# Kernel tuning notes

Measured on AMD Instinct MI355X. Metric: run time of the kernel, lower is better.

Reference implementation:

```python
import jax, jax.numpy as jnp
import numpy as np

B = 36          # fixed batch_size in source
T = 60          # time_window
DECAY = 0.3     # LIAF default decay
THRESH = 0.5    # LIAF default firing threshold


def conv3x3(x, W, b):
    # x: [B,C,H,W], W: [O,C,3,3], padding=1, stride=1
    y = jax.lax.conv_general_dilated(x, W, (1, 1), [(1, 1), (1, 1)],
                                     dimension_numbers=('NCHW', 'OIHW', 'NCHW'))
    return y + b[None, :, None, None]


def avgpool2(x):
    # 2x2 average pool, stride 2
    b, c, h, w = x.shape
    return x.reshape(b, c, h // 2, 2, w // 2, 2).mean(axis=(3, 5))


def liaf(u, spike, mem):
    # leaky-integrate with spike-gated reset, analog (ReLU) fire
    mem = mem * DECAY * (1.0 - spike) + u
    new_spike = (mem > THRESH).astype(mem.dtype)
    out = jax.nn.relu(mem)
    return new_spike, mem, out


def setup_inputs() -> dict:
    key = jax.random.key(0)
    ks = jax.random.split(key, 8)
    # DVS event frames in [0,3) so the >1 binarization keeps ~2/3 of pixels
    data = (jax.random.uniform(ks[0], (B, 2, 32, 32, T)) * 3.0).astype(jnp.float32)

    def w(k, shape, fan_in):
        return (jax.random.normal(k, shape) * (1.0 / np.sqrt(fan_in))).astype(jnp.float32)

    return dict(
        data=data,
        win=T,
        W0=w(ks[1], (64, 2, 3, 3), 2 * 9), b0=jnp.zeros((64,), jnp.float32),
        W1=w(ks[2], (128, 64, 3, 3), 64 * 9), b1=jnp.zeros((128,), jnp.float32),
        W2=w(ks[3], (128, 128, 3, 3), 128 * 9), b2=jnp.zeros((128,), jnp.float32),
        Wf1=w(ks[4], (256, 8192), 8192), bf1=jnp.zeros((256,), jnp.float32),
        Wf2=w(ks[5], (11, 256), 256), bf2=jnp.zeros((11,), jnp.float32),
    )


def reference(data, W0, b0, W1, b1, W2, b2, Wf1, bf1, Wf2, bf2, win):
    dtype = data.dtype
    z = lambda s: jnp.zeros(s, dtype)
    # (spike, mem) pairs for every LIAF cell + output-spike accumulator
    state0 = (
        (z((B, 64, 32, 32)), z((B, 64, 32, 32))),   # c0
        (z((B, 128, 32, 32)), z((B, 128, 32, 32))), # c1
        (z((B, 128, 16, 16)), z((B, 128, 16, 16))), # p1
        (z((B, 128, 16, 16)), z((B, 128, 16, 16))), # c2
        (z((B, 128, 8, 8)), z((B, 128, 8, 8))),     # p2
        (z((B, 256)), z((B, 256))),                 # h1
        (z((B, 11)), z((B, 11))),                   # h2
        z((B, 11)),                                 # sum of analog outputs
    )
    xs = jnp.moveaxis(data, -1, 0)[:win]

    def step(st, xt):
        c0, c1, p1, c2, p2, h1, h2, acc = st
        x = (xt > 1.0).astype(dtype)  # binarize accumulated frame
        s, m, out = liaf(conv3x3(x, W0, b0), *c0); c0 = (s, m)
        s, m, out = liaf(conv3x3(out, W1, b1), *c1); c1 = (s, m)
        s, m, out = liaf(avgpool2(out), *p1); p1 = (s, m)
        s, m, out = liaf(conv3x3(out, W2, b2), *c2); c2 = (s, m)
        s, m, out = liaf(avgpool2(out), *p2); p2 = (s, m)
        out = out.reshape(B, -1)  # [B, 8*8*128]
        s, m, out = liaf(out @ Wf1.T + bf1, *h1); h1 = (s, m)
        s, m, out = liaf(out @ Wf2.T + bf2, *h2); h2 = (s, m)
        return (c0, c1, p1, c2, p2, h1, h2, acc + out), None

    st_f, _ = jax.lax.scan(step, state0, xs)
    return st_f[-1] / T
```

## Files before the change

### kernel.cpp

```cpp
#include <hip/hip_runtime.h>

#define NB 36
#define NT 60

typedef __attribute__((ext_vector_type(8))) short short8;
typedef __attribute__((ext_vector_type(4))) float f32x4;

struct Params {
  const float *data;
  const float *W0, *b0, *W1, *b1, *W2, *b2, *Wf1, *bf1, *Wf2, *bf2;
  float *xb, *w0t;
  unsigned short *w1h, *w1l, *w2h, *w2l;
  unsigned int *xhl, *p1hl;
  float *outp2, *u1s;
  float *dm0, *dm1, *dmp1, *dm2, *dmp2, *dmh1, *dmh2;
  float *acc;
  float *zbase; int zn4;
};

__device__ __forceinline__ unsigned short bf16_rne(float v){
  unsigned int bits = __float_as_uint(v);
  unsigned int r = bits + 0x7FFFu + ((bits >> 16) & 1u);
  return (unsigned short)(r >> 16);
}
__device__ __forceinline__ unsigned int bf16pack(float v){
  unsigned short h = bf16_rne(v);
  float hf = __uint_as_float((unsigned int)h << 16);
  unsigned short l = bf16_rne(v - hf);
  return (unsigned int)h | ((unsigned int)l << 16);
}
__device__ __forceinline__ void unpack8(const unsigned int* q, short8& h8, short8& l8){
  unsigned int u[8];
  *(uint4*)&u[0] = *(const uint4*)q;
  *(uint4*)&u[4] = *(const uint4*)(q+4);
  #pragma unroll
  for(int i=0;i<8;i++){
    h8[i] = (short)(u[i] & 0xffffu);
    l8[i] = (short)(u[i] >> 16);
  }
}

__global__ void __launch_bounds__(256) k_prep(Params p){
  int gt  = blockIdx.x*256 + threadIdx.x;
  int STR = gridDim.x*256;
  if(gt < NB*11) p.acc[gt] = 0.f;
  for(int i=gt; i<p.zn4; i+=STR) ((float4*)p.zbase)[i] = make_float4(0.f,0.f,0.f,0.f);
  const int PLANE = 34*34;
  for(int i=gt; i<NT*NB*2*PLANE; i+=STR){
    int t   = i / (NB*2*PLANE);
    int rem = i % (NB*2*PLANE);
    int bc  = rem / PLANE;
    int pix = rem % PLANE;
    int ph = pix/34, pw = pix%34;
    float v = 0.f;
    if(ph>=1 && ph<=32 && pw>=1 && pw<=32){
      float d = p.data[((size_t)bc*1024 + (ph-1)*32 + (pw-1))*NT + t];
      v = (d > 1.0f) ? 1.0f : 0.0f;
    }
    p.xb[i] = v;
  }
  for(int i=gt; i<2*9*64; i+=STR){
    int co=i%64, rr=i/64; p.w0t[i] = p.W0[(co*2 + rr/9)*9 + rr%9];
  }
  for(int i=gt; i<128*576; i+=STR){
    int co = i/576, k = i%576;
    int cin = k/9, dd = k%9;
    unsigned int pk = bf16pack(p.W1[(co*64+cin)*9 + dd]);
    p.w1h[i]=(unsigned short)(pk&0xffffu); p.w1l[i]=(unsigned short)(pk>>16);
  }
  for(int i=gt; i<128*1152; i+=STR){
    int co = i/1152, k = i%1152;
    int cin = k/9, dd = k%9;
    unsigned int pk = bf16pack(p.W2[(co*128+cin)*9 + dd]);
    p.w2h[i]=(unsigned short)(pk&0xffffu); p.w2l[i]=(unsigned short)(pk>>16);
  }
}

template<int Cin,int Cout,int HW,int CO,int PX,int TY,int CS>
__global__ void __launch_bounds__(HW*TY)
k_conv0(const float* __restrict__ x, const float* __restrict__ wt,
        const float* __restrict__ bias, float* __restrict__ dm,
        unsigned int* __restrict__ outhl,
        const float* __restrict__ u1s, const float* __restrict__ bf1,
        const float* __restrict__ Wf2, const float* __restrict__ bf2,
        float* __restrict__ dmh1, float* __restrict__ dmh2,
        float* __restrict__ accv, int do_fc2)
{
  const int NCOG = Cout/CO;
  const int TH   = PX*TY;
  const int NHG  = HW/TH;
  const int NH4  = CO/4;
  const int NTHL = HW*TY;
  const int PIN  = HW+2;
  const int XR   = PX+2;
  int tile = blockIdx.x;
  int tid  = threadIdx.x;

  __shared__ __align__(16) float wl[CS*9*CO];
  __shared__ float xs[256];

  if(do_fc2 && tile < NB){
    int b = tile;
    int o = tid;
    float u = bf1[o];
    const float* pu = u1s + (size_t)b*256 + o;
    #pragma unroll
    for(int s=0;s<32;s++) u += pu[(size_t)s*NB*256];
    int idx = b*256 + o;
    float mem = dmh1[idx] + u;
    float xo = mem > 0.f ? mem : 0.f;
    dmh1[idx] = (mem > 0.5f) ? 0.f : 0.3f*mem;
    xs[o] = xo;
    __syncthreads();
    int w2id = o >> 6, ln = o & 63;
    for(int oo=w2id; oo<11; oo+=4){
      const float* wr = Wf2 + oo*256;
      float s = xs[ln]*wr[ln] + xs[ln+64]*wr[ln+64]
              + xs[ln+128]*wr[ln+128] + xs[ln+192]*wr[ln+192];
      #pragma unroll
      for(int off=32; off>0; off>>=1) s += __shfl_down(s, off, 64);
      if(ln==0){
        int i2 = b*11 + oo;
        float m2 = dmh2[i2] + s + bf2[oo];
        float ov = m2 > 0.f ? m2 : 0.f;
        dmh2[i2] = (m2 > 0.5f) ? 0.f : 0.3f*m2;
        accv[i2] += ov * (1.0f/60.0f);
      }
    }
  }

  int cog = tile % NCOG;
  int hg  = (tile/NCOG) % NHG;
  int b   = tile/(NCOG*NHG);
  int w0  = tid % HW;
  int ty  = tid / HW;
  int h0  = hg*TH + ty*PX;

  float accs[PX][CO];
  #pragma unroll
  for(int p=0;p<PX;p++)
    #pragma unroll
    for(int c=0;c<CO;c++) accs[p][c]=0.f;

  for(int cs=0; cs<Cin; cs+=CS){
    __syncthreads();
    for(int j=tid; j<CS*9*CO; j+=NTHL){
      int c  = j % CO;
      int rr = j / CO;
      wl[j] = wt[(cs*9 + rr)*Cout + cog*CO + c];
    }
    __syncthreads();

    for(int lc=0; lc<CS; lc++){
      const float* xc = x + ((size_t)b*Cin + cs + lc)*PIN*PIN + (size_t)h0*PIN + w0;
      float xv[XR][3];
      #pragma unroll
      for(int r=0;r<XR;r++)
        #pragma unroll
        for(int c=0;c<3;c++) xv[r][c] = xc[(size_t)r*PIN + c];
      const float4* w4 = (const float4*)(wl + lc*9*CO);
      #pragma unroll
      for(int dh=0;dh<3;dh++){
        #pragma unroll
        for(int g=0;g<NH4;g++){
          float4 wa = w4[(dh*3+0)*NH4+g];
          float4 wb = w4[(dh*3+1)*NH4+g];
          float4 wc = w4[(dh*3+2)*NH4+g];
          const float* A  = (const float*)&wa;
          const float* Bp = (const float*)&wb;
          const float* Cp = (const float*)&wc;
          #pragma unroll
          for(int cc=0;cc<4;cc++){
            #pragma unroll
            for(int px=0;px<PX;px++)
              accs[px][g*4+cc] += A[cc]*xv[px+dh][0] + Bp[cc]*xv[px+dh][1] + Cp[cc]*xv[px+dh][2];
          }
        }
      }
    }
  }

  int co0 = cog*CO;
  #pragma unroll
  for(int co=0; co<CO; co++){
    float bsv = bias[co0+co];
    const int OS = HW + 2;
    size_t plane = (size_t)(b*Cout + co0+co)*OS*OS;
    #pragma unroll
    for(int px=0; px<PX; px++){
      size_t idx = plane + (size_t)(h0+px+1)*OS + w0 + 1;
      float mem = dm[idx] + accs[px][co] + bsv;
      float ov = mem > 0.f ? mem : 0.f;
      dm[idx]  = (mem > 0.5f) ? 0.f : 0.3f*mem;
      outhl[idx] = bf16pack(ov);
    }
  }
}

__global__ void __launch_bounds__(256, 4)
k_conv1(const unsigned int* __restrict__ xhl,
        const unsigned short* __restrict__ w1h, const unsigned short* __restrict__ w1l,
        const float* __restrict__ bias, float* __restrict__ dm,
        float* __restrict__ dmp, unsigned int* __restrict__ p1hl)
{
  __shared__ __align__(16) unsigned int ldsu[5376];
  unsigned short* Ah = (unsigned short*)ldsu;
  unsigned short* Al = (unsigned short*)(ldsu + 1280);
  unsigned int*   Xp = ldsu + 2560;

  int bid = blockIdx.x;
  int cog = bid & 1;
  int pxg = (bid>>1) & 15;
  int b   = bid >> 5;
  int tid = threadIdx.x;
  int wv  = tid >> 6, lane = tid & 63;
  int wm = wv & 1, wn = wv >> 1;
  int n = lane & 15, quad = lane >> 4;
  int r0 = pxg*2;

  f32x4 acc[2][2];
  #pragma unroll
  for(int mo=0;mo<2;mo++)
    #pragma unroll
    for(int no=0;no<2;no++) acc[mo][no] = (f32x4){0.f,0.f,0.f,0.f};

  int aco = tid >> 2;
  int aq  = tid & 3;
  const unsigned short* whp = w1h + (size_t)(cog*64 + aco)*576 + aq*8;
  const unsigned short* wlp = w1l + (size_t)(cog*64 + aco)*576 + aq*8;
  int sk  = tid >> 3;
  int pxq = tid & 7;
  int srow = pxq >> 2;
  int scol = (pxq & 3) * 8;
  int rA   = pxq * 8;
  int skx  = sk ^ (((pxq >> 1) & 3) << 3);

  uint4 wha = *(const uint4*)(whp);
  uint4 wla = *(const uint4*)(wlp);
  unsigned int tmp[8];
  {
    int cin = sk / 9;
    int dd  = sk - cin*9;
    int dh = dd/3, dw = dd - dh*3;
    const unsigned int* sx = xhl + ((size_t)(b*64 + cin)*34 + (r0 + srow + dh))*34 + scol + dw;
    #pragma unroll
    for(int i=0;i<8;i++) tmp[i] = sx[i];
  }

  for(int ch=0; ch<18; ch++){
    __syncthreads();
    *(uint4*)&Ah[aco*40 + aq*8] = wha;
    *(uint4*)&Al[aco*40 + aq*8] = wla;
    #pragma unroll
    for(int i=0;i<8;i++) Xp[(rA+i)*44 + skx] = tmp[i];
    __syncthreads();

    if(ch+1 < 18){
      int k0n = (ch+1)*32;
      wha = *(const uint4*)(whp + k0n);
      wla = *(const uint4*)(wlp + k0n);
      int kg = k0n + sk;
      int cin = kg / 9;
      int dd  = kg - cin*9;
      int dh = dd/3, dw = dd - dh*3;
      const unsigned int* sx = xhl + ((size_t)(b*64 + cin)*34 + (r0 + srow + dh))*34 + scol + dw;
      #pragma unroll
      for(int i=0;i<8;i++) tmp[i] = sx[i];
    }

    short8 ahf[2], alf[2];
    #pragma unroll
    for(int mo=0;mo<2;mo++){
      int row = wm*32 + mo*16 + n;
      ahf[mo] = *(const short8*)&Ah[row*40 + quad*8];
      alf[mo] = *(const short8*)&Al[row*40 + quad*8];
    }
    #pragma unroll
    for(int no=0;no<2;no++){
      int prow = no*32 + wn*16 + n;
      int cb = ((quad ^ (no*2 + wn)) & 3) * 8;
      short8 xhf, xlf;
      unpack8(&Xp[prow*44 + cb], xhf, xlf);
      #pragma unroll
      for(int mo=0;mo<2;mo++){
        acc[mo][no] = __builtin_amdgcn_mfma_f32_16x16x32_bf16(ahf[mo], xhf, acc[mo][no],0,0,0);
        acc[mo][no] = __builtin_amdgcn_mfma_f32_16x16x32_bf16(ahf[mo], xlf, acc[mo][no],0,0,0);
        acc[mo][no] = __builtin_amdgcn_mfma_f32_16x16x32_bf16(alf[mo], xhf, acc[mo][no],0,0,0);
      }
    }
  }

  #pragma unroll
  for(int mo=0;mo<2;mo++){
    #pragma unroll
    for(int reg=0;reg<4;reg++){
      int co = cog*64 + wm*32 + mo*16 + quad*4 + reg;
      float bsv = bias[co];
      float o[2];
      #pragma unroll
      for(int no=0;no<2;no++){
        int r = r0 + no;
        int c = wn*16 + n;
        size_t idx = (((size_t)b*128 + co)*32 + r)*32 + c;
        float mem = dm[idx] + acc[mo][no][reg] + bsv;
        o[no] = mem > 0.f ? mem : 0.f;
        dm[idx] = (mem > 0.5f) ? 0.f : 0.3f*mem;
      }
      float s = o[0] + o[1];
      s += __shfl_xor(s, 1, 64);
      if((n&1)==0){
        int pr = pxg;
        int pc = wn*8 + (n>>1);
        size_t pidx = (((size_t)b*128 + co)*18 + pr+1)*18 + pc+1;
        float pm = dmp[pidx] + s*0.25f;
        float pv = pm > 0.f ? pm : 0.f;
        dmp[pidx] = (pm > 0.5f) ? 0.f : 0.3f*pm;
        p1hl[pidx] = bf16pack(pv);
      }
    }
  }
}

__global__ void __launch_bounds__(256, 4)
k_conv2(const unsigned int* __restrict__ xhl,
        const unsigned short* __restrict__ w2h, const unsigned short* __restrict__ w2l,
        const float* __restrict__ bias, float* __restrict__ dm,
        float* __restrict__ dmp, float* __restrict__ outp)
{
  __shared__ __align__(16) unsigned int ldsu[3968];
  unsigned short* Ah = (unsigned short*)ldsu;
  unsigned short* Al = (unsigned short*)(ldsu + 1280);
  unsigned int*   Xp = ldsu + 2560;

  int bid = blockIdx.x;
  int cog = bid & 1;
  int pxg = (bid>>1) & 7;
  int b   = bid >> 4;
  int tid = threadIdx.x;
  int wv  = tid >> 6, lane = tid & 63;
  int wm = wv & 1, wn = wv >> 1;
  int n = lane & 15, quad = lane >> 4;
  int r0 = pxg*2;

  f32x4 acc2[2];
  #pragma unroll
  for(int mo=0;mo<2;mo++) acc2[mo] = (f32x4){0.f,0.f,0.f,0.f};

  int aco = tid >> 2;
  int aq  = tid & 3;
  const unsigned short* whp = w2h + (size_t)(cog*64 + aco)*1152 + aq*8;
  const unsigned short* wlp = w2l + (size_t)(cog*64 + aco)*1152 + aq*8;
  int sk  = tid >> 3;
  int pxq = tid & 7;
  int srow = pxq >> 2;
  int scol = (pxq & 3) * 4;
  int rA   = pxq * 4;
  int skx  = sk ^ ((pxq >> 2) << 3);

  uint4 wha = *(const uint4*)(whp);
  uint4 wla = *(const uint4*)(wlp);
  unsigned int tmp[4];
  {
    int cin = sk / 9;
    int dd  = sk - cin*9;
    int dh = dd/3, dw = dd - dh*3;
    const unsigned int* sx = xhl + ((size_t)(b*128 + cin)*18 + (r0 + srow + dh))*18 + scol + dw;
    #pragma unroll
    for(int i=0;i<4;i++) tmp[i] = sx[i];
  }

  for(int ch=0; ch<36; ch++){
    __syncthreads();
    *(uint4*)&Ah[aco*40 + aq*8] = wha;
    *(uint4*)&Al[aco*40 + aq*8] = wla;
    #pragma unroll
    for(int i=0;i<4;i++) Xp[(rA+i)*44 + skx] = tmp[i];
    __syncthreads();

    if(ch+1 < 36){
      int k0n = (ch+1)*32;
      wha = *(const uint4*)(whp + k0n);
      wla = *(const uint4*)(wlp + k0n);
      int kg = k0n + sk;
      int cin = kg / 9;
      int dd  = kg - cin*9;
      int dh = dd/3, dw = dd - dh*3;
      const unsigned int* sx = xhl + ((size_t)(b*128 + cin)*18 + (r0 + srow + dh))*18 + scol + dw;
      #pragma unroll
      for(int i=0;i<4;i++) tmp[i] = sx[i];
    }

    short8 ahf[2], alf[2];
    #pragma unroll
    for(int mo=0;mo<2;mo++){
      int row = wm*32 + mo*16 + n;
      ahf[mo] = *(const short8*)&Ah[row*40 + quad*8];
      alf[mo] = *(const short8*)&Al[row*40 + quad*8];
    }
    {
      int prow = (n>>3)*16 + wn*8 + (n&7);
      int cb = ((quad ^ (n>>3)) & 3) * 8;
      short8 xhf, xlf;
      unpack8(&Xp[prow*44 + cb], xhf, xlf);
      #pragma unroll
      for(int mo=0;mo<2;mo++){
        acc2[mo] = __builtin_amdgcn_mfma_f32_16x16x32_bf16(ahf[mo], xhf, acc2[mo],0,0,0);
        acc2[mo] = __builtin_amdgcn_mfma_f32_16x16x32_bf16(ahf[mo], xlf, acc2[mo],0,0,0);
        acc2[mo] = __builtin_amdgcn_mfma_f32_16x16x32_bf16(alf[mo], xhf, acc2[mo],0,0,0);
      }
    }
  }

  #pragma unroll
  for(int mo=0;mo<2;mo++){
    #pragma unroll
    for(int reg=0;reg<4;reg++){
      int co = cog*64 + wm*32 + mo*16 + quad*4 + reg;
      float bsv = bias[co];
      int r = r0 + (n>>3);
      int c = wn*8 + (n&7);
      size_t idx = (((size_t)b*128 + co)*16 + r)*16 + c;
      float mem = dm[idx] + acc2[mo][reg] + bsv;
      float o = mem > 0.f ? mem : 0.f;
      dm[idx] = (mem > 0.5f) ? 0.f : 0.3f*mem;
      float s = o;
      s += __shfl_xor(s, 8, 64);
      s += __shfl_xor(s, 1, 64);
      if((n & 9) == 0){
        int pr = pxg;
        int pc = wn*4 + ((n&7)>>1);
        size_t pidx = (((size_t)b*128 + co)*8 + pr)*8 + pc;
        float pm = dmp[pidx] + s*0.25f;
        outp[pidx] = pm > 0.f ? pm : 0.f;
        dmp[pidx]  = (pm > 0.5f) ? 0.f : 0.3f*pm;
      }
    }
  }
}

__global__ void __launch_bounds__(256)
k_fc1(const float* __restrict__ X, const float* __restrict__ Wf,
      float* __restrict__ u1s){
  __shared__ __align__(16) float lds[4896];
  float* Wl = lds;
  float* Xl = lds + 32*68;
  const int tid = threadIdx.x;
  int ot = blockIdx.x & 7, ks = blockIdx.x >> 3;
  int o0 = ot*32, k0 = ks*256;
  int w_id = tid >> 6, lane = tid & 63;
  int o_l = lane & 7, bg = lane >> 3;
  float acc[4][5];
  #pragma unroll
  for(int i=0;i<4;i++)
    #pragma unroll
    for(int j=0;j<5;j++) acc[i][j]=0.f;

  for(int c=0; c<4; c++){
    int kb = k0 + c*64;
    __syncthreads();
    for(int idx=tid; idx<512; idx+=256){
      int r = idx >> 4, j = idx & 15;
      *(float4*)&Wl[r*68 + j*4] = *(const float4*)&Wf[(size_t)(o0+r)*8192 + kb + j*4];
    }
    for(int idx=tid; idx<640; idx+=256){
      int r = idx >> 4, j = idx & 15;
      float4 v = make_float4(0.f,0.f,0.f,0.f);
      if(r < NB) v = *(const float4*)&X[(size_t)r*8192 + kb + j*4];
      *(float4*)&Xl[r*68 + j*4] = v;
    }
    __syncthreads();
    #pragma unroll
    for(int c4=0; c4<4; c4++){
      int g = w_id*4 + c4;
      float4 wv[4], xv[5];
      #pragma unroll
      for(int oi=0;oi<4;oi++) wv[oi] = *(const float4*)&Wl[(o_l+8*oi)*68 + g*4];
      #pragma unroll
      for(int bi=0;bi<5;bi++) xv[bi] = *(const float4*)&Xl[(bg*5+bi)*68 + g*4];
      #pragma unroll
      for(int oi=0;oi<4;oi++)
        #pragma unroll
        for(int bi=0;bi<5;bi++)
          acc[oi][bi] += wv[oi].x*xv[bi].x + wv[oi].y*xv[bi].y
                       + wv[oi].z*xv[bi].z + wv[oi].w*xv[bi].w;
    }
  }
  __syncthreads();
  if(w_id > 0){
    float* r = lds + ((w_id-1)*64 + lane)*20;
    #pragma unroll
    for(int oi=0;oi<4;oi++)
      #pragma unroll
      for(int bi=0;bi<5;bi++) r[oi*5+bi] = acc[oi][bi];
  }
  __syncthreads();
  if(w_id == 0){
    #pragma unroll
    for(int wv=0;wv<3;wv++){
      float* r = lds + (wv*64 + lane)*20;
      #pragma unroll
      for(int oi=0;oi<4;oi++)
        #pragma unroll
        for(int bi=0;bi<5;bi++) acc[oi][bi] += r[oi*5+bi];
    }
    #pragma unroll
    for(int bi=0;bi<5;bi++){
      int b = bg*5 + bi;
      if(b < NB){
        #pragma unroll
        for(int oi=0;oi<4;oi++)
          u1s[((size_t)ks*NB + b)*256 + o0 + o_l + 8*oi] = acc[oi][bi];
      }
    }
  }
}

__global__ void __launch_bounds__(256)
k_fc2(const float* __restrict__ u1s, const float* __restrict__ bf1,
      const float* __restrict__ Wf2, const float* __restrict__ bf2,
      float* __restrict__ dmh1, float* __restrict__ dmh2, float* __restrict__ acc){
  __shared__ float xs[256];
  int b = blockIdx.x;
  int o = threadIdx.x;
  float u = bf1[o];
  const float* p = u1s + (size_t)b*256 + o;
  #pragma unroll
  for(int s=0;s<32;s++) u += p[(size_t)s*NB*256];
  int idx = b*256 + o;
  float mem = dmh1[idx] + u;
  float xo = mem > 0.f ? mem : 0.f;
  dmh1[idx] = (mem > 0.5f) ? 0.f : 0.3f*mem;
  xs[o] = xo;
  __syncthreads();
  int w_id = o >> 6, lane = o & 63;
  for(int oo=w_id; oo<11; oo+=4){
    const float* wr = Wf2 + oo*256;
    float s = xs[lane]*wr[lane] + xs[lane+64]*wr[lane+64]
            + xs[lane+128]*wr[lane+128] + xs[lane+192]*wr[lane+192];
    #pragma unroll
    for(int off=32; off>0; off>>=1) s += __shfl_down(s, off, 64);
    if(lane==0){
      int i2 = b*11 + oo;
      float m2 = dmh2[i2] + s + bf2[oo];
      float ov = m2 > 0.f ? m2 : 0.f;
      dmh2[i2] = (m2 > 0.5f) ? 0.f : 0.3f*m2;
      acc[i2] += ov * (1.0f/60.0f);
    }
  }
}

extern "C" void kernel_launch(void* const* d_in, const int* in_sizes, int n_in,
                              void* d_out, int out_size, void* d_ws, size_t ws_size,
                              hipStream_t stream) {
  Params p;
  p.data = (const float*)d_in[0];
  p.W0  = (const float*)d_in[2];  p.b0  = (const float*)d_in[3];
  p.W1  = (const float*)d_in[4];  p.b1  = (const float*)d_in[5];
  p.W2  = (const float*)d_in[6];  p.b2  = (const float*)d_in[7];
  p.Wf1 = (const float*)d_in[8];  p.bf1 = (const float*)d_in[9];
  p.Wf2 = (const float*)d_in[10]; p.bf2 = (const float*)d_in[11];
  p.acc = (float*)d_out;

  float* ws = (float*)d_ws;
  const size_t S_XB    = (size_t)NT*NB*2*34*34;
  const size_t S_W0T   = 2*9*64;
  const size_t S_W1S   = 128*576/2;
  const size_t S_W2S   = 128*1152/2;
  const size_t S_XHL   = (size_t)NB*64*34*34;
  const size_t S_P1HL  = (size_t)NB*128*18*18;
  const size_t S_OP2   = (size_t)NB*128*8*8;
  const size_t S_U1S   = (size_t)32*NB*256;
  const size_t S_DM0   = (size_t)NB*64*34*34;
  const size_t S_DM1   = (size_t)NB*128*32*32;
  const size_t S_DMP1  = (size_t)NB*128*18*18;
  const size_t S_DM2   = (size_t)NB*128*16*16;
  const size_t S_DMP2  = S_OP2;
  const size_t S_OH1   = (size_t)NB*256;

  p.xb    = ws;  ws += S_XB;
  p.w0t   = ws;  ws += S_W0T;
  p.w1h   = (unsigned short*)ws;  ws += S_W1S;
  p.w1l   = (unsigned short*)ws;  ws += S_W1S;
  p.w2h   = (unsigned short*)ws;  ws += S_W2S;
  p.w2l   = (unsigned short*)ws;  ws += S_W2S;
  p.zbase = ws;
  p.xhl   = (unsigned int*)ws;    ws += S_XHL;
  p.p1hl  = (unsigned int*)ws;    ws += S_P1HL;
  p.outp2 = ws;  ws += S_OP2;
  p.u1s   = ws;  ws += S_U1S;
  p.dm0   = ws;  ws += S_DM0;
  p.dm1   = ws;  ws += S_DM1;
  p.dmp1  = ws;  ws += S_DMP1;
  p.dm2   = ws;  ws += S_DM2;
  p.dmp2  = ws;  ws += S_DMP2;
  p.dmh1  = ws;  ws += S_OH1;
  p.dmh2  = ws;  ws += (size_t)NB*11;
  p.zn4   = (int)((ws - p.zbase) / 4);

  k_prep<<<dim3(1024), dim3(256), 0, stream>>>(p);
  for(int t=0; t<NT; t++){
    const float* xt = p.xb + (size_t)t*NB*2*34*34;
    k_conv0<2,64,32,8,4,8,2><<<dim3(288), dim3(256), 0, stream>>>(
        xt, p.w0t, p.b0, p.dm0, p.xhl,
        p.u1s, p.bf1, p.Wf2, p.bf2, p.dmh1, p.dmh2, p.acc, t > 0 ? 1 : 0);
    k_conv1<<<dim3(1152), dim3(256), 0, stream>>>(
        p.xhl, p.w1h, p.w1l, p.b1, p.dm1, p.dmp1, p.p1hl);
    k_conv2<<<dim3(576), dim3(256), 0, stream>>>(
        p.p1hl, p.w2h, p.w2l, p.b2, p.dm2, p.dmp2, p.outp2);
    k_fc1<<<dim3(256), dim3(256), 0, stream>>>(p.outp2, p.Wf1, p.u1s);
  }
  k_fc2<<<dim3(36), dim3(256), 0, stream>>>(p.u1s, p.bf1, p.Wf2, p.bf2,
                                            p.dmh1, p.dmh2, p.acc);
}
```

Baseline: 5.805 ms.

## Fuse next-step conv0 and fc2 into conv2 launch to cut per-step kernels

Moves conv0 for timestep t+1 and fc2 for timestep t-1 into extra blocks of the conv2 kernel, so each timestep needs three launches instead of four. Conv0 for t=0 runs once before the loop. This is meant to cut launch overhead and fill idle CUs with independent work alongside conv2. It depends on conv1 having finished reading xhl before conv0 overwrites it, which holds because conv1 is the previous launch. The fused kernel also carries the register budget of the mixed block roles.

New measurement: 5.259 ms. -9.4%, faster.

```diff
diff --git a/kernel.cpp b/kernel.cpp
--- a/kernel.cpp
+++ b/kernel.cpp
@@ -80,11 +80,7 @@
 __global__ void __launch_bounds__(HW*TY)
 k_conv0(const float* __restrict__ x, const float* __restrict__ wt,
         const float* __restrict__ bias, float* __restrict__ dm,
-        unsigned int* __restrict__ outhl,
-        const float* __restrict__ u1s, const float* __restrict__ bf1,
-        const float* __restrict__ Wf2, const float* __restrict__ bf2,
-        float* __restrict__ dmh1, float* __restrict__ dmh2,
-        float* __restrict__ accv, int do_fc2)
+        unsigned int* __restrict__ outhl)
 {
   const int NCOG = Cout/CO;
   const int TH   = PX*TY;
@@ -95,46 +91,14 @@
   const int XR   = PX+2;
   int tile = blockIdx.x;
   int tid  = threadIdx.x;
-
-  __shared__ __align__(16) float wl[CS*9*CO];
-  __shared__ float xs[256];
-
-  if(do_fc2 && tile < NB){
-    int b = tile;
-    int o = tid;
-    float u = bf1[o];
-    const float* pu = u1s + (size_t)b*256 + o;
-    #pragma unroll
-    for(int s=0;s<32;s++) u += pu[(size_t)s*NB*256];
-    int idx = b*256 + o;
-    float mem = dmh1[idx] + u;
-    float xo = mem > 0.f ? mem : 0.f;
-    dmh1[idx] = (mem > 0.5f) ? 0.f : 0.3f*mem;
-    xs[o] = xo;
-    __syncthreads();
-    int w2id = o >> 6, ln = o & 63;
-    for(int oo=w2id; oo<11; oo+=4){
-      const float* wr = Wf2 + oo*256;
-      float s = xs[ln]*wr[ln] + xs[ln+64]*wr[ln+64]
-              + xs[ln+128]*wr[ln+128] + xs[ln+192]*wr[ln+192];
-      #pragma unroll
-      for(int off=32; off>0; off>>=1) s += __shfl_down(s, off, 64);
-      if(ln==0){
-        int i2 = b*11 + oo;
-        float m2 = dmh2[i2] + s + bf2[oo];
-        float ov = m2 > 0.f ? m2 : 0.f;
-        dmh2[i2] = (m2 > 0.5f) ? 0.f : 0.3f*m2;
-        accv[i2] += ov * (1.0f/60.0f);
-      }
-    }
-  }
-
   int cog = tile % NCOG;
   int hg  = (tile/NCOG) % NHG;
   int b   = tile/(NCOG*NHG);
   int w0  = tid % HW;
   int ty  = tid / HW;
   int h0  = hg*TH + ty*PX;
+
+  __shared__ __align__(16) float wl[CS*9*CO];
 
   float accs[PX][CO];
   #pragma unroll
@@ -322,21 +286,131 @@
 }
 
 __global__ void __launch_bounds__(256, 4)
-k_conv2(const unsigned int* __restrict__ xhl,
-        const unsigned short* __restrict__ w2h, const unsigned short* __restrict__ w2l,
-        const float* __restrict__ bias, float* __restrict__ dm,
-        float* __restrict__ dmp, float* __restrict__ outp)
+k_x2(const unsigned int* __restrict__ p1hl,
+     const unsigned short* __restrict__ w2h, const unsigned short* __restrict__ w2l,
+     const float* __restrict__ bias2, float* __restrict__ dm2,
+     float* __restrict__ dmp2, float* __restrict__ outp,
+     const float* __restrict__ xnext, const float* __restrict__ w0t,
+     const float* __restrict__ bias0, float* __restrict__ dm0,
+     unsigned int* __restrict__ xhl, int do_c0,
+     const float* __restrict__ u1s, const float* __restrict__ bf1,
+     const float* __restrict__ Wf2, const float* __restrict__ bf2,
+     float* __restrict__ dmh1, float* __restrict__ dmh2,
+     float* __restrict__ accv, int do_fc2)
 {
   __shared__ __align__(16) unsigned int ldsu[3968];
+  const int tid = threadIdx.x;
+  int bid = blockIdx.x;
+
+  if(bid >= 864){
+    if(!do_fc2) return;
+    float* xs = (float*)ldsu;
+    int b = bid - 864;
+    int o = tid;
+    float u = bf1[o];
+    const float* pu = u1s + (size_t)b*256 + o;
+    #pragma unroll
+    for(int s=0;s<32;s++) u += pu[(size_t)s*NB*256];
+    int idx = b*256 + o;
+    float mem = dmh1[idx] + u;
+    float xo = mem > 0.f ? mem : 0.f;
+    dmh1[idx] = (mem > 0.5f) ? 0.f : 0.3f*mem;
+    xs[o] = xo;
+    __syncthreads();
+    int w_id = o >> 6, ln = o & 63;
+    for(int oo=w_id; oo<11; oo+=4){
+      const float* wr = Wf2 + oo*256;
+      float s = xs[ln]*wr[ln] + xs[ln+64]*wr[ln+64]
+              + xs[ln+128]*wr[ln+128] + xs[ln+192]*wr[ln+192];
+      #pragma unroll
+      for(int off=32; off>0; off>>=1) s += __shfl_down(s, off, 64);
+      if(ln==0){
+        int i2 = b*11 + oo;
+        float m2 = dmh2[i2] + s + bf2[oo];
+        float ov = m2 > 0.f ? m2 : 0.f;
+        dmh2[i2] = (m2 > 0.5f) ? 0.f : 0.3f*m2;
+        accv[i2] += ov * (1.0f/60.0f);
+      }
+    }
+    return;
+  }
+
+  if(bid >= 576){
+    if(!do_c0) return;
+    float* wl = (float*)ldsu;
+    int tile = bid - 576;
+    int cog = tile & 7;
+    int b   = tile >> 3;
+    int w0  = tid & 31;
+    int ty  = tid >> 5;
+    int h0  = ty*4;
+
+    float accs[4][8];
+    #pragma unroll
+    for(int p=0;p<4;p++)
+      #pragma unroll
+      for(int c=0;c<8;c++) accs[p][c]=0.f;
+
+    if(tid < 144){
+      int c  = tid % 8;
+      int rr = tid / 8;
+      wl[tid] = w0t[rr*64 + cog*8 + c];
+    }
+    __syncthreads();
+
+    #pragma unroll
+    for(int lc=0; lc<2; lc++){
+      const float* xc = xnext + ((size_t)b*2 + lc)*34*34 + (size_t)h0*34 + w0;
+      float xv[6][3];
+      #pragma unroll
+      for(int r=0;r<6;r++)
+        #pragma unroll
+        for(int c=0;c<3;c++) xv[r][c] = xc[(size_t)r*34 + c];
+      const float4* w4 = (const float4*)(wl + lc*72);
+      #pragma unroll
+      for(int dh=0;dh<3;dh++){
+        #pragma unroll
+        for(int g=0;g<2;g++){
+          float4 wa = w4[(dh*3+0)*2+g];
+          float4 wb = w4[(dh*3+1)*2+g];
+          float4 wc = w4[(dh*3+2)*2+g];
+          const float* A  = (const float*)&wa;
+          const float* Bp = (const float*)&wb;
+          const float* Cp = (const float*)&wc;
+          #pragma unroll
+          for(int cc=0;cc<4;cc++){
+            #pragma unroll
+            for(int px=0;px<4;px++)
+              accs[px][g*4+cc] += A[cc]*xv[px+dh][0] + Bp[cc]*xv[px+dh][1] + Cp[cc]*xv[px+dh][2];
+          }
+        }
+      }
+    }
+
+    int co0 = cog*8;
+    #pragma unroll
+    for(int co=0; co<8; co++){
+      float bsv = bias0[co0+co];
+      size_t plane = (size_t)(b*64 + co0+co)*34*34;
+      #pragma unroll
+      for(int px=0; px<4; px++){
+        size_t idx = plane + (size_t)(h0+px+1)*34 + w0 + 1;
+        float mem = dm0[idx] + accs[px][co] + bsv;
+        float ov = mem > 0.f ? mem : 0.f;
+        dm0[idx]  = (mem > 0.5f) ? 0.f : 0.3f*mem;
+        xhl[idx] = bf16pack(ov);
+      }
+    }
+    return;
+  }
+
   unsigned short* Ah = (unsigned short*)ldsu;
   unsigned short* Al = (unsigned short*)(ldsu + 1280);
   unsigned int*   Xp = ldsu + 2560;
 
-  int bid = blockIdx.x;
   int cog = bid & 1;
   int pxg = (bid>>1) & 7;
   int b   = bid >> 4;
-  int tid = threadIdx.x;
   int wv  = tid >> 6, lane = tid & 63;
   int wm = wv & 1, wn = wv >> 1;
   int n = lane & 15, quad = lane >> 4;
@@ -364,7 +438,7 @@
     int cin = sk / 9;
     int dd  = sk - cin*9;
     int dh = dd/3, dw = dd - dh*3;
-    const unsigned int* sx = xhl + ((size_t)(b*128 + cin)*18 + (r0 + srow + dh))*18 + scol + dw;
+    const unsigned int* sx = p1hl + ((size_t)(b*128 + cin)*18 + (r0 + srow + dh))*18 + scol + dw;
     #pragma unroll
     for(int i=0;i<4;i++) tmp[i] = sx[i];
   }
@@ -385,7 +459,7 @@
       int cin = kg / 9;
       int dd  = kg - cin*9;
       int dh = dd/3, dw = dd - dh*3;
-      const unsigned int* sx = xhl + ((size_t)(b*128 + cin)*18 + (r0 + srow + dh))*18 + scol + dw;
+      const unsigned int* sx = p1hl + ((size_t)(b*128 + cin)*18 + (r0 + srow + dh))*18 + scol + dw;
       #pragma unroll
       for(int i=0;i<4;i++) tmp[i] = sx[i];
     }
@@ -416,13 +490,13 @@
     #pragma unroll
     for(int reg=0;reg<4;reg++){
       int co = cog*64 + wm*32 + mo*16 + quad*4 + reg;
-      float bsv = bias[co];
+      float bsv = bias2[co];
       int r = r0 + (n>>3);
       int c = wn*8 + (n&7);
       size_t idx = (((size_t)b*128 + co)*16 + r)*16 + c;
-      float mem = dm[idx] + acc2[mo][reg] + bsv;
+      float mem = dm2[idx] + acc2[mo][reg] + bsv;
       float o = mem > 0.f ? mem : 0.f;
-      dm[idx] = (mem > 0.5f) ? 0.f : 0.3f*mem;
+      dm2[idx] = (mem > 0.5f) ? 0.f : 0.3f*mem;
       float s = o;
       s += __shfl_xor(s, 8, 64);
       s += __shfl_xor(s, 1, 64);
@@ -430,9 +504,9 @@
         int pr = pxg;
         int pc = wn*4 + ((n&7)>>1);
         size_t pidx = (((size_t)b*128 + co)*8 + pr)*8 + pc;
-        float pm = dmp[pidx] + s*0.25f;
+        float pm = dmp2[pidx] + s*0.25f;
         outp[pidx] = pm > 0.f ? pm : 0.f;
-        dmp[pidx]  = (pm > 0.5f) ? 0.f : 0.3f*pm;
+        dmp2[pidx]  = (pm > 0.5f) ? 0.f : 0.3f*pm;
       }
     }
   }
@@ -598,15 +672,16 @@
   p.zn4   = (int)((ws - p.zbase) / 4);
 
   k_prep<<<dim3(1024), dim3(256), 0, stream>>>(p);
+  k_conv0<2,64,32,8,4,8,2><<<dim3(288), dim3(256), 0, stream>>>(
+      p.xb, p.w0t, p.b0, p.dm0, p.xhl);
   for(int t=0; t<NT; t++){
-    const float* xt = p.xb + (size_t)t*NB*2*34*34;
-    k_conv0<2,64,32,8,4,8,2><<<dim3(288), dim3(256), 0, stream>>>(
-        xt, p.w0t, p.b0, p.dm0, p.xhl,
-        p.u1s, p.bf1, p.Wf2, p.bf2, p.dmh1, p.dmh2, p.acc, t > 0 ? 1 : 0);
     k_conv1<<<dim3(1152), dim3(256), 0, stream>>>(
         p.xhl, p.w1h, p.w1l, p.b1, p.dm1, p.dmp1, p.p1hl);
-    k_conv2<<<dim3(576), dim3(256), 0, stream>>>(
-        p.p1hl, p.w2h, p.w2l, p.b2, p.dm2, p.dmp2, p.outp2);
+    const float* xnext = p.xb + (size_t)(t+1)*NB*2*34*34;
+    k_x2<<<dim3(900), dim3(256), 0, stream>>>(
+        p.p1hl, p.w2h, p.w2l, p.b2, p.dm2, p.dmp2, p.outp2,
+        xnext, p.w0t, p.b0, p.dm0, p.xhl, t < NT-1 ? 1 : 0,
+        p.u1s, p.bf1, p.Wf2, p.bf2, p.dmh1, p.dmh2, p.acc, t > 0 ? 1 : 0);
     k_fc1<<<dim3(256), dim3(256), 0, stream>>>(p.outp2, p.Wf1, p.u1s);
   }
   k_fc2<<<dim3(36), dim3(256), 0, stream>>>(p.u1s, p.bf1, p.Wf2, p.bf2,
```
